# Performance work log

Hardware: AMD Instinct MI355X
Metric: run time of the kernel (lower is better)

Reference implementation:

```python
import jax, jax.numpy as jnp
import numpy as np

ALPHA = 0.25
GAMMA = 2.0
DELTA = 0.5
BREAK_W = 1.0
REG_W = 1.0
CLASS_WEIGHT_TABLE = jnp.array([1.0, 4.0, 3.0, 2.0], dtype=jnp.float32)  # classes 0..3
LOG_CLAMP = -100.0  # torch BCELoss clamps log terms at -100

B, T = 2048, 16384


def setup_inputs() -> dict:
    key = jax.random.key(0)
    k1, k2, k3, k4 = jax.random.split(key, 4)
    break_predictions = jax.random.uniform(k1, (B, T), dtype=jnp.float32)
    regression_predictions = jax.random.uniform(k2, (B, T), dtype=jnp.float32) * 3.0
    break_targets = jax.random.uniform(k3, (B, T), dtype=jnp.float32)
    regression_targets = jax.random.uniform(k4, (B, T), dtype=jnp.float32) * 3.0
    return {
        "break_predictions": break_predictions,
        "regression_predictions": regression_predictions,
        "break_targets": break_targets,
        "regression_targets": regression_targets,
    }


def _bce(p, t):
    # torch BCELoss: mean of -(t*log(p) + (1-t)*log(1-p)), logs clamped at -100
    log_p = jnp.maximum(jnp.log(p), LOG_CLAMP)
    log_1p = jnp.maximum(jnp.log1p(-p), LOG_CLAMP)
    return jnp.mean(-(t * log_p + (1.0 - t) * log_1p))


def _duration_aware_focal(y_pred, y_true):
    y_pred = y_pred.reshape(-1)
    y_true = y_true.reshape(-1)
    # class-weight gather: round + clamp to [0,3], index a 4-entry table
    cls_idx = jnp.clip(jnp.round(y_true), 0.0, 3.0).astype(jnp.int32)
    weights = CLASS_WEIGHT_TABLE[cls_idx]
    d = jnp.abs(y_pred - y_true)
    focal = jnp.clip(d / DELTA, 0.0, 1.0) ** GAMMA
    # smooth L1 with beta=DELTA
    base = jnp.where(d < DELTA, 0.5 * d * d / DELTA, d - 0.5 * DELTA)
    return jnp.mean(ALPHA * focal * base * weights)


def reference(break_predictions, regression_predictions, break_targets, regression_targets):
    bt = jnp.clip(break_targets, 0.0, 1.0)
    bp = jnp.clip(break_predictions, 0.0, 1.0)
    break_loss = _bce(bp, bt)
    regression_loss = _duration_aware_focal(regression_predictions, regression_targets)
    total = BREAK_W * break_loss + REG_W * regression_loss
    return (total, break_loss, regression_loss)
```

## Files before the change

kernel.cpp:

```cpp
#include <hip/hip_runtime.h>


constexpr int BLOCK = 256;
constexpr int GRID  = 2048;

__device__ __forceinline__ void accum_elem(float pv, float tv, float qv, float sv,
                                           float& accB, float& accR) {
    constexpr float LN2 = 0.6931471805599453f;
    float pc = fminf(fmaxf(pv, 0.0f), 1.0f);
    float tc = fminf(fmaxf(tv, 0.0f), 1.0f);
    float lp  = fmaxf(__log2f(pc)        * LN2, -100.0f);
    float l1p = fmaxf(__log2f(1.0f - pc) * LN2, -100.0f);
    accB -= tc * lp + (1.0f - tc) * l1p;
    float d = fabsf(qv - sv);
    float f = fminf(d + d, 1.0f);
    float base = (d < 0.5f) ? (d * d) : (d - 0.25f);
    float r = fminf(fmaxf(__builtin_rintf(sv), 0.0f), 3.0f);
    float w = (r == 0.0f) ? 1.0f : (r == 1.0f) ? 4.0f : (r == 2.0f) ? 3.0f : 2.0f;
    accR += 0.25f * (f * f) * base * w;
}

__global__ __launch_bounds__(BLOCK) void partial_kernel(
    const float4* __restrict__ bp4, const float4* __restrict__ rp4,
    const float4* __restrict__ bt4, const float4* __restrict__ rt4,
    float* __restrict__ partials, int n4, int n)
{
    float accB = 0.0f, accR = 0.0f;
    const int stride = gridDim.x * blockDim.x;
    for (int i = blockIdx.x * blockDim.x + threadIdx.x; i < n4; i += stride) {
        float4 p = bp4[i];
        float4 t = bt4[i];
        float4 q = rp4[i];
        float4 s = rt4[i];
        accum_elem(p.x, t.x, q.x, s.x, accB, accR);
        accum_elem(p.y, t.y, q.y, s.y, accB, accR);
        accum_elem(p.z, t.z, q.z, s.z, accB, accR);
        accum_elem(p.w, t.w, q.w, s.w, accB, accR);
    }
    if (blockIdx.x == 0) {
        const float* bp = (const float*)bp4;
        const float* bt = (const float*)bt4;
        const float* rp = (const float*)rp4;
        const float* rt = (const float*)rt4;
        for (int i = n4 * 4 + threadIdx.x; i < n; i += BLOCK)
            accum_elem(bp[i], bt[i], rp[i], rt[i], accB, accR);
    }
    #pragma unroll
    for (int off = 32; off > 0; off >>= 1) {
        accB += __shfl_down(accB, off, 64);
        accR += __shfl_down(accR, off, 64);
    }
    __shared__ float sB[BLOCK / 64], sR[BLOCK / 64];
    const int lane = threadIdx.x & 63;
    const int wid  = threadIdx.x >> 6;
    if (lane == 0) { sB[wid] = accB; sR[wid] = accR; }
    __syncthreads();
    if (threadIdx.x == 0) {
        float b = 0.0f, r = 0.0f;
        #pragma unroll
        for (int w = 0; w < BLOCK / 64; ++w) { b += sB[w]; r += sR[w]; }
        partials[blockIdx.x]        = b;
        partials[GRID + blockIdx.x] = r;
    }
}

__global__ __launch_bounds__(BLOCK) void final_kernel(
    const float* __restrict__ partials, float* __restrict__ out, double invN)
{
    double accB = 0.0, accR = 0.0;
    for (int i = threadIdx.x; i < GRID; i += BLOCK) {
        accB += (double)partials[i];
        accR += (double)partials[GRID + i];
    }
    #pragma unroll
    for (int off = 32; off > 0; off >>= 1) {
        accB += __shfl_down(accB, off, 64);
        accR += __shfl_down(accR, off, 64);
    }
    __shared__ double dB[BLOCK / 64], dR[BLOCK / 64];
    const int lane = threadIdx.x & 63;
    const int wid  = threadIdx.x >> 6;
    if (lane == 0) { dB[wid] = accB; dR[wid] = accR; }
    __syncthreads();
    if (threadIdx.x == 0) {
        double b = 0.0, r = 0.0;
        #pragma unroll
        for (int w = 0; w < BLOCK / 64; ++w) { b += dB[w]; r += dR[w]; }
        const double bm = b * invN;
        const double rm = r * invN;
        out[0] = (float)(bm + rm);
        out[1] = (float)bm;
        out[2] = (float)rm;
    }
}

extern "C" void kernel_launch(void* const* d_in, const int* in_sizes, int n_in,
                              void* d_out, int out_size, void* d_ws, size_t ws_size,
                              hipStream_t stream) {
    const float* bp = (const float*)d_in[0];
    const float* rp = (const float*)d_in[1];
    const float* bt = (const float*)d_in[2];
    const float* rt = (const float*)d_in[3];
    const int n  = in_sizes[0];
    const int n4 = n / 4;
    float* partials = (float*)d_ws;

    partial_kernel<<<GRID, BLOCK, 0, stream>>>(
        (const float4*)bp, (const float4*)rp, (const float4*)bt, (const float4*)rt,
        partials, n4, n);
    final_kernel<<<1, BLOCK, 0, stream>>>(partials, (float*)d_out, 1.0 / (double)n);
}
```

Before: 101.0 us.

## Split BCE and focal reductions across separate block halves and hoist constant scales

Result: no change. 102.4 us (+1.4%).

```diff
diff --git a/kernel.cpp b/kernel.cpp
--- a/kernel.cpp
+++ b/kernel.cpp
@@ -2,22 +2,25 @@
 
 
 constexpr int BLOCK = 256;
-constexpr int GRID  = 2048;
+constexpr int HGRID = 2048;
+constexpr int GRID  = 2 * HGRID;
 
-__device__ __forceinline__ void accum_elem(float pv, float tv, float qv, float sv,
-                                           float& accB, float& accR) {
-    constexpr float LN2 = 0.6931471805599453f;
+__device__ __forceinline__ void bce_elem(float pv, float tv, float& acc) {
+    constexpr float CLAMP2 = -144.26950408889634f;
     float pc = fminf(fmaxf(pv, 0.0f), 1.0f);
     float tc = fminf(fmaxf(tv, 0.0f), 1.0f);
-    float lp  = fmaxf(__log2f(pc)        * LN2, -100.0f);
-    float l1p = fmaxf(__log2f(1.0f - pc) * LN2, -100.0f);
-    accB -= tc * lp + (1.0f - tc) * l1p;
+    float lp  = fmaxf(__log2f(pc),        CLAMP2);
+    float l1p = fmaxf(__log2f(1.0f - pc), CLAMP2);
+    acc -= l1p + tc * (lp - l1p);
+}
+
+__device__ __forceinline__ void focal_elem(float qv, float sv, float& acc) {
     float d = fabsf(qv - sv);
     float f = fminf(d + d, 1.0f);
     float base = (d < 0.5f) ? (d * d) : (d - 0.25f);
     float r = fminf(fmaxf(__builtin_rintf(sv), 0.0f), 3.0f);
     float w = (r == 0.0f) ? 1.0f : (r == 1.0f) ? 4.0f : (r == 2.0f) ? 3.0f : 2.0f;
-    accR += 0.25f * (f * f) * base * w;
+    acc += (f * f) * base * w;
 }
 
 __global__ __launch_bounds__(BLOCK) void partial_kernel(
@@ -25,42 +28,57 @@
     const float4* __restrict__ bt4, const float4* __restrict__ rt4,
     float* __restrict__ partials, int n4, int n)
 {
-    float accB = 0.0f, accR = 0.0f;
-    const int stride = gridDim.x * blockDim.x;
-    for (int i = blockIdx.x * blockDim.x + threadIdx.x; i < n4; i += stride) {
-        float4 p = bp4[i];
-        float4 t = bt4[i];
-        float4 q = rp4[i];
-        float4 s = rt4[i];
-        accum_elem(p.x, t.x, q.x, s.x, accB, accR);
-        accum_elem(p.y, t.y, q.y, s.y, accB, accR);
-        accum_elem(p.z, t.z, q.z, s.z, accB, accR);
-        accum_elem(p.w, t.w, q.w, s.w, accB, accR);
+    const int stride = HGRID * BLOCK;
+    float a0 = 0.0f, a1 = 0.0f;
+    const bool isB = (blockIdx.x < HGRID);
+    const int  vb  = isB ? blockIdx.x : blockIdx.x - HGRID;
+
+    if (isB) {
+        for (int i = vb * BLOCK + threadIdx.x; i < n4; i += stride) {
+            float4 p = bp4[i];
+            float4 t = bt4[i];
+            bce_elem(p.x, t.x, a0);
+            bce_elem(p.y, t.y, a1);
+            bce_elem(p.z, t.z, a0);
+            bce_elem(p.w, t.w, a1);
+        }
+        if (vb == 0) {
+            const float* bp = (const float*)bp4;
+            const float* bt = (const float*)bt4;
+            for (int k = n4 * 4 + threadIdx.x; k < n; k += BLOCK)
+                bce_elem(bp[k], bt[k], a0);
+        }
+    } else {
+        for (int i = vb * BLOCK + threadIdx.x; i < n4; i += stride) {
+            float4 q = rp4[i];
+            float4 s = rt4[i];
+            focal_elem(q.x, s.x, a0);
+            focal_elem(q.y, s.y, a1);
+            focal_elem(q.z, s.z, a0);
+            focal_elem(q.w, s.w, a1);
+        }
+        if (vb == 0) {
+            const float* rp = (const float*)rp4;
+            const float* rt = (const float*)rt4;
+            for (int k = n4 * 4 + threadIdx.x; k < n; k += BLOCK)
+                focal_elem(rp[k], rt[k], a0);
+        }
     }
-    if (blockIdx.x == 0) {
-        const float* bp = (const float*)bp4;
-        const float* bt = (const float*)bt4;
-        const float* rp = (const float*)rp4;
-        const float* rt = (const float*)rt4;
-        for (int i = n4 * 4 + threadIdx.x; i < n; i += BLOCK)
-            accum_elem(bp[i], bt[i], rp[i], rt[i], accB, accR);
-    }
+
+    float acc = a0 + a1;
     #pragma unroll
-    for (int off = 32; off > 0; off >>= 1) {
-        accB += __shfl_down(accB, off, 64);
-        accR += __shfl_down(accR, off, 64);
-    }
-    __shared__ float sB[BLOCK / 64], sR[BLOCK / 64];
+    for (int off = 32; off > 0; off >>= 1)
+        acc += __shfl_down(acc, off, 64);
+    __shared__ float sA[BLOCK / 64];
     const int lane = threadIdx.x & 63;
     const int wid  = threadIdx.x >> 6;
-    if (lane == 0) { sB[wid] = accB; sR[wid] = accR; }
+    if (lane == 0) sA[wid] = acc;
     __syncthreads();
     if (threadIdx.x == 0) {
-        float b = 0.0f, r = 0.0f;
+        float v = 0.0f;
         #pragma unroll
-        for (int w = 0; w < BLOCK / 64; ++w) { b += sB[w]; r += sR[w]; }
-        partials[blockIdx.x]        = b;
-        partials[GRID + blockIdx.x] = r;
+        for (int w = 0; w < BLOCK / 64; ++w) v += sA[w];
+        partials[blockIdx.x] = v;
     }
 }
 
@@ -68,9 +86,9 @@
     const float* __restrict__ partials, float* __restrict__ out, double invN)
 {
     double accB = 0.0, accR = 0.0;
-    for (int i = threadIdx.x; i < GRID; i += BLOCK) {
+    for (int i = threadIdx.x; i < HGRID; i += BLOCK) {
         accB += (double)partials[i];
-        accR += (double)partials[GRID + i];
+        accR += (double)partials[HGRID + i];
     }
     #pragma unroll
     for (int off = 32; off > 0; off >>= 1) {
@@ -86,8 +104,8 @@
         double b = 0.0, r = 0.0;
         #pragma unroll
         for (int w = 0; w < BLOCK / 64; ++w) { b += dB[w]; r += dR[w]; }
-        const double bm = b * invN;
-        const double rm = r * invN;
+        const double bm = b * 0.6931471805599453 * invN;
+        const double rm = r * 0.25 * invN;
         out[0] = (float)(bm + rm);
         out[1] = (float)bm;
         out[2] = (float)rm;
```
